# Kernel optimization log

Hardware: AMD Instinct MI355X
Metric: run time of the kernel (lower is better)

The kernel has to match this reference:

```python
import jax, jax.numpy as jnp
import numpy as np

EPS = 1e-6      # torch F.pairwise_distance default eps (added to the difference)
MARGIN = 1.0

def _cdist_eps(a, b):
    # Exact ||a_i - b_j + eps||_2 via expansion:
    # ||a-b+eps||^2 = ||a||^2 + ||b||^2 - 2 a.b + 2*eps*(sum(a)-sum(b)) + D*eps^2
    D = a.shape[-1]
    sq = (jnp.sum(a * a, axis=1)[:, None]
          + jnp.sum(b * b, axis=1)[None, :]
          - 2.0 * (a @ b.T)
          + 2.0 * EPS * (jnp.sum(a, axis=1)[:, None] - jnp.sum(b, axis=1)[None, :])
          + D * EPS * EPS)
    return jnp.sqrt(jnp.maximum(sq, 0.0))

def setup_inputs() -> dict:
    key = jax.random.key(0)
    k1, k2, k3 = jax.random.split(key, 3)
    B, D = 4096, 1024
    return {
        'anchor_embeddings': jax.random.normal(k1, (B, D), dtype=jnp.float32),
        'positive_embeddings': jax.random.normal(k2, (B, D), dtype=jnp.float32),
        'negative_embeddings': jax.random.normal(k3, (B, D), dtype=jnp.float32),
    }

def reference(anchor_embeddings, positive_embeddings, negative_embeddings):
    a, p, n = anchor_embeddings, positive_embeddings, negative_embeddings
    # per-row anchor-positive and anchor-negative distances
    d_ap = jnp.linalg.norm(a - p + EPS, axis=-1)          # [B]
    d_an_row = jnp.linalg.norm(a - n + EPS, axis=-1)      # [B]

    # hardest negative: for each anchor, max over negatives with dist < d_ap[i], else 0
    dan_mat = _cdist_eps(a, n)                            # [B, B]
    mask_n = dan_mat < d_ap[:, None]
    hard_n = jnp.where(mask_n.any(axis=1),
                       jnp.max(jnp.where(mask_n, dan_mat, -jnp.inf), axis=1),
                       0.0)
    d_an = jnp.mean(hard_n)                               # scalar

    # hardest positive: for each anchor, min over positives with dist > d(a_i, n_i), else 0
    dpp_mat = _cdist_eps(a, p)                            # [B, B]
    mask_p = dpp_mat > d_an_row[:, None]
    hard_p = jnp.where(mask_p.any(axis=1),
                       jnp.min(jnp.where(mask_p, dpp_mat, jnp.inf), axis=1),
                       0.0)
    d_pp = jnp.mean(hard_p)                               # scalar

    loss = jnp.mean(jnp.clip(d_ap - 0.5 * d_pp - 0.5 * d_an + MARGIN, 0.0, None))
    return loss
```

## Files before the change

kernel.cpp:

```cpp
#include <hip/hip_runtime.h>


#define NB 4096
#define DIM 1024
#define EPSF 1e-6f
#define D_EPS2 (1024.0f * 1e-6f * 1e-6f)

#define BM 128
#define BK 64

typedef __bf16  bf16x8 __attribute__((ext_vector_type(8)));
typedef float   f32x4  __attribute__((ext_vector_type(4)));

__device__ __forceinline__ unsigned short f2bf(float x) {
    unsigned u = __float_as_uint(x);
    u += 0x7FFFu + ((u >> 16) & 1u);
    return (unsigned short)(u >> 16);
}

__device__ __forceinline__ void g2l16(const unsigned short* g, unsigned short* l) {
    __builtin_amdgcn_global_load_lds(
        (const __attribute__((address_space(1))) unsigned int*)g,
        (__attribute__((address_space(3))) unsigned int*)l, 16, 0, 0);
}


__global__ __launch_bounds__(256) void row_stats_kernel(
    const float* __restrict__ a, const float* __restrict__ p,
    const float* __restrict__ n,
    unsigned short* __restrict__ abf, unsigned short* __restrict__ pbf,
    unsigned short* __restrict__ nbf, float* __restrict__ stats)
{
    const int t    = threadIdx.x;
    const int wave = t >> 6, lane = t & 63;
    const int row  = blockIdx.x * 4 + wave;
    const size_t base = (size_t)row * DIM;

    const float4* a4 = (const float4*)(a + base);
    const float4* p4 = (const float4*)(p + base);
    const float4* n4 = (const float4*)(n + base);

    float v[8] = {0,0,0,0,0,0,0,0};
#pragma unroll
    for (int c = 0; c < 4; c++) {
        const int idx = c * 64 + lane;
        const float4 va = a4[idx];
        const float4 vp = p4[idx];
        const float4 vn = n4[idx];
        const float fa[4] = {va.x, va.y, va.z, va.w};
        const float fp[4] = {vp.x, vp.y, vp.z, vp.w};
        const float fn[4] = {vn.x, vn.y, vn.z, vn.w};
#pragma unroll
        for (int e = 0; e < 4; e++) {
            v[0] += fa[e];           v[1] += fa[e] * fa[e];
            v[2] += fp[e];           v[3] += fp[e] * fp[e];
            v[4] += fn[e];           v[5] += fn[e] * fn[e];
            float dp = fa[e] - fp[e] + EPSF;  v[6] += dp * dp;
            float dn = fa[e] - fn[e] + EPSF;  v[7] += dn * dn;
        }
        ushort4 ba, bp, bn;
        ba.x = f2bf(fa[0]); ba.y = f2bf(fa[1]); ba.z = f2bf(fa[2]); ba.w = f2bf(fa[3]);
        bp.x = f2bf(fp[0]); bp.y = f2bf(fp[1]); bp.z = f2bf(fp[2]); bp.w = f2bf(fp[3]);
        bn.x = f2bf(fn[0]); bn.y = f2bf(fn[1]); bn.z = f2bf(fn[2]); bn.w = f2bf(fn[3]);
        ((ushort4*)(abf + base))[idx] = ba;
        ((ushort4*)(pbf + base))[idx] = bp;
        ((ushort4*)(nbf + base))[idx] = bn;
    }

#pragma unroll
    for (int m = 32; m >= 1; m >>= 1)
#pragma unroll
        for (int q = 0; q < 8; q++) v[q] += __shfl_xor(v[q], m);

    if (lane == 0) {
        stats[0 * NB + row] = v[1] + 2.0f * EPSF * v[0] + D_EPS2;
        stats[1 * NB + row] = v[5] - 2.0f * EPSF * v[4];
        stats[2 * NB + row] = v[3] - 2.0f * EPSF * v[2];
        stats[3 * NB + row] = sqrtf(v[6]);
        stats[4 * NB + row] = sqrtf(v[7]);
        ((unsigned*)stats)[5 * NB + row] = 0u;
        ((unsigned*)stats)[6 * NB + row] = 0x7f800000u;
    }
}

__global__ __launch_bounds__(256, 2) void gemm_mask_kernel(
    const unsigned short* __restrict__ Abf,
    const unsigned short* __restrict__ Nbf,
    const unsigned short* __restrict__ Pbf,
    float* __restrict__ stats)
{
    const int i0 = blockIdx.x * BM;
    const int j0 = blockIdx.y * BM;

    __shared__ unsigned short sA[BM * BK];
    __shared__ unsigned short sN[BM * BK];
    __shared__ unsigned short sP[BM * BK];

    const int t    = threadIdx.x;
    const int wave = t >> 6, lane = t & 63;
    const int wm   = wave >> 1, wn = wave & 1;
    const int quad = lane >> 4, lrow = lane & 15;

    const int srow = lane >> 3;
    const int kch  = ((lane & 7) ^ srow) * 8;
    const unsigned short* gA = Abf + (size_t)(i0 + wave * 32 + srow) * DIM + kch;
    const unsigned short* gN = Nbf + (size_t)(j0 + wave * 32 + srow) * DIM + kch;
    const unsigned short* gP = Pbf + (size_t)(j0 + wave * 32 + srow) * DIM + kch;
    unsigned short* lA = sA + (wave * 32) * BK;
    unsigned short* lN = sN + (wave * 32) * BK;
    unsigned short* lP = sP + (wave * 32) * BK;

    const int rsw0 = ((0 * 4 + quad) ^ (lrow & 7)) * 8;
    const int rsw1 = ((1 * 4 + quad) ^ (lrow & 7)) * 8;
    const unsigned short* pa  = sA + (wm * 64 + lrow) * BK;
    const unsigned short* pbn = sN + (wn * 64 + lrow) * BK;
    const unsigned short* pbp = sP + (wn * 64 + lrow) * BK;

    f32x4 accN[4][4], accP[4][4];
#pragma unroll
    for (int im = 0; im < 4; im++)
#pragma unroll
        for (int jn = 0; jn < 4; jn++) {
            accN[im][jn] = (f32x4)(0.0f);
            accP[im][jn] = (f32x4)(0.0f);
        }

    for (int kt = 0; kt < DIM; kt += BK) {
        __syncthreads();
#pragma unroll
        for (int g = 0; g < 4; g++) {
            g2l16(gA + (size_t)kt + g * 8 * DIM, lA + g * 8 * BK);
            g2l16(gN + (size_t)kt + g * 8 * DIM, lN + g * 8 * BK);
            g2l16(gP + (size_t)kt + g * 8 * DIM, lP + g * 8 * BK);
        }
        __syncthreads();

#pragma unroll
        for (int half = 0; half < 2; half++) {
            const int rsw = half ? rsw1 : rsw0;
            bf16x8 afr[4], bn_fr[4], bp_fr[4];
#pragma unroll
            for (int im = 0; im < 4; im++)
                afr[im] = *(const bf16x8*)(pa + im * 16 * BK + rsw);
#pragma unroll
            for (int jn = 0; jn < 4; jn++) {
                bn_fr[jn] = *(const bf16x8*)(pbn + jn * 16 * BK + rsw);
                bp_fr[jn] = *(const bf16x8*)(pbp + jn * 16 * BK + rsw);
            }
#pragma unroll
            for (int im = 0; im < 4; im++)
#pragma unroll
                for (int jn = 0; jn < 4; jn++) {
                    accN[im][jn] = __builtin_amdgcn_mfma_f32_16x16x32_bf16(
                        afr[im], bn_fr[jn], accN[im][jn], 0, 0, 0);
                    accP[im][jn] = __builtin_amdgcn_mfma_f32_16x16x32_bf16(
                        afr[im], bp_fr[jn], accP[im][jn], 0, 0, 0);
                }
        }
    }

    const float* __restrict__ base_a = stats + 0 * NB;
    const float* __restrict__ cn_v   = stats + 1 * NB;
    const float* __restrict__ cp_v   = stats + 2 * NB;
    const float* __restrict__ d_ap   = stats + 3 * NB;
    const float* __restrict__ d_an   = stats + 4 * NB;
    unsigned* __restrict__ hard_n = ((unsigned*)stats) + 5 * NB;
    unsigned* __restrict__ hard_p = ((unsigned*)stats) + 6 * NB;

#pragma unroll
    for (int im = 0; im < 4; im++) {
#pragma unroll
        for (int r = 0; r < 4; r++) {
            const int gi = i0 + wm * 64 + im * 16 + quad * 4 + r;
            const float cutN = d_ap[gi];
            const float cutP = d_an[gi];
            const float bi   = base_a[gi];
            float bestN = 0.0f;
            float bestP = __uint_as_float(0x7f800000u);
#pragma unroll
            for (int jn = 0; jn < 4; jn++) {
                const int gj = j0 + wn * 64 + jn * 16 + lrow;
                const float dN = sqrtf(fmaxf(bi + cn_v[gj] - 2.0f * accN[im][jn][r], 0.0f));
                const float dP = sqrtf(fmaxf(bi + cp_v[gj] - 2.0f * accP[im][jn][r], 0.0f));
                if (dN < cutN && dN > bestN) bestN = dN;
                if (dP > cutP && dP < bestP) bestP = dP;
            }
#pragma unroll
            for (int m = 1; m < 16; m <<= 1) {
                bestN = fmaxf(bestN, __shfl_xor(bestN, m));
                bestP = fminf(bestP, __shfl_xor(bestP, m));
            }
            if (lrow == 0) {
                const unsigned bn_ = __float_as_uint(bestN);
                const unsigned bp_ = __float_as_uint(bestP);
                if (bn_ != 0u)          atomicMax(hard_n + gi, bn_);
                if (bp_ != 0x7f800000u) atomicMin(hard_p + gi, bp_);
            }
        }
    }
}

__global__ __launch_bounds__(1024) void finalize_kernel(
    const float* __restrict__ stats, float* __restrict__ out)
{
    const unsigned* hard_n = ((const unsigned*)stats) + 5 * NB;
    const unsigned* hard_p = ((const unsigned*)stats) + 6 * NB;
    const float*    d_ap   = stats + 3 * NB;
    const int t = threadIdx.x;
    const int wave = t >> 6, lane = t & 63;
    __shared__ float pn[16], pp[16];
    __shared__ float s_dan, s_dpp;

    float sn = 0.0f, sp = 0.0f;
    for (int i = t; i < NB; i += 1024) {
        sn += __uint_as_float(hard_n[i]);
        const unsigned hp = hard_p[i];
        if (hp != 0x7f800000u) sp += __uint_as_float(hp);
    }
#pragma unroll
    for (int m = 32; m >= 1; m >>= 1) {
        sn += __shfl_xor(sn, m);
        sp += __shfl_xor(sp, m);
    }
    if (lane == 0) { pn[wave] = sn; pp[wave] = sp; }
    __syncthreads();
    if (t == 0) {
        float an = 0.0f, ap = 0.0f;
#pragma unroll
        for (int w = 0; w < 16; w++) { an += pn[w]; ap += pp[w]; }
        s_dan = an / (float)NB;
        s_dpp = ap / (float)NB;
    }
    __syncthreads();
    const float dan = s_dan, dpp = s_dpp;

    float accv = 0.0f;
    for (int i = t; i < NB; i += 1024)
        accv += fmaxf(d_ap[i] - 0.5f * dpp - 0.5f * dan + 1.0f, 0.0f);
#pragma unroll
    for (int m = 32; m >= 1; m >>= 1) accv += __shfl_xor(accv, m);
    if (lane == 0) pn[wave] = accv;
    __syncthreads();
    if (t == 0) {
        float s = 0.0f;
#pragma unroll
        for (int w = 0; w < 16; w++) s += pn[w];
        out[0] = s / (float)NB;
    }
}

extern "C" void kernel_launch(void* const* d_in, const int* in_sizes, int n_in,
                              void* d_out, int out_size, void* d_ws, size_t ws_size,
                              hipStream_t stream) {
    const float* a = (const float*)d_in[0];
    const float* p = (const float*)d_in[1];
    const float* n = (const float*)d_in[2];
    float* out = (float*)d_out;

    unsigned short* abf = (unsigned short*)d_ws;
    unsigned short* pbf = abf + (size_t)NB * DIM;
    unsigned short* nbf = pbf + (size_t)NB * DIM;
    float* stats = (float*)(nbf + (size_t)NB * DIM);

    row_stats_kernel<<<NB / 4, 256, 0, stream>>>(a, p, n, abf, pbf, nbf, stats);

    dim3 grid(NB / BM, NB / BM);
    gemm_mask_kernel<<<grid, 256, 0, stream>>>(abf, nbf, pbf, stats);

    finalize_kernel<<<1, 1024, 0, stream>>>(stats, out);
}
```

Measured before the change: 183.4 us.

## Split fused N/P GEMM into separate blocks, load A directly, compare squared distances

The fused kernel that computed both anchor-negative and anchor-positive accumulators per block is split so that each block handles only one of N or P, selected by a new grid dimension. This halves the accumulator registers and LDS per block and raises the launch-bounds occupancy target. The A fragments are now loaded straight from global memory into registers instead of being staged through LDS. Masking compares squared distances against squared cutoffs, and the sqrt moves into finalize. The costs are A being read twice, uncoalesced global loads of A, and possible rounding differences at the threshold from comparing squares.

```diff
diff --git a/kernel.cpp b/kernel.cpp
--- a/kernel.cpp
+++ b/kernel.cpp
@@ -83,18 +83,18 @@
     }
 }
 
-__global__ __launch_bounds__(256, 2) void gemm_mask_kernel(
+__global__ __launch_bounds__(256, 3) void gemm_mask_kernel(
     const unsigned short* __restrict__ Abf,
     const unsigned short* __restrict__ Nbf,
     const unsigned short* __restrict__ Pbf,
     float* __restrict__ stats)
 {
-    const int i0 = blockIdx.x * BM;
-    const int j0 = blockIdx.y * BM;
-
-    __shared__ unsigned short sA[BM * BK];
-    __shared__ unsigned short sN[BM * BK];
-    __shared__ unsigned short sP[BM * BK];
+    const int  isP = blockIdx.x;
+    const int  j0  = blockIdx.y * BM;
+    const int  i0  = blockIdx.z * BM;
+    const unsigned short* __restrict__ Bmat = isP ? Pbf : Nbf;
+
+    __shared__ unsigned short sB[BM * BK];
 
     const int t    = threadIdx.x;
     const int wave = t >> 6, lane = t & 63;
@@ -103,98 +103,82 @@
 
     const int srow = lane >> 3;
     const int kch  = ((lane & 7) ^ srow) * 8;
-    const unsigned short* gA = Abf + (size_t)(i0 + wave * 32 + srow) * DIM + kch;
-    const unsigned short* gN = Nbf + (size_t)(j0 + wave * 32 + srow) * DIM + kch;
-    const unsigned short* gP = Pbf + (size_t)(j0 + wave * 32 + srow) * DIM + kch;
-    unsigned short* lA = sA + (wave * 32) * BK;
-    unsigned short* lN = sN + (wave * 32) * BK;
-    unsigned short* lP = sP + (wave * 32) * BK;
-
-    const int rsw0 = ((0 * 4 + quad) ^ (lrow & 7)) * 8;
-    const int rsw1 = ((1 * 4 + quad) ^ (lrow & 7)) * 8;
-    const unsigned short* pa  = sA + (wm * 64 + lrow) * BK;
-    const unsigned short* pbn = sN + (wn * 64 + lrow) * BK;
-    const unsigned short* pbp = sP + (wn * 64 + lrow) * BK;
-
-    f32x4 accN[4][4], accP[4][4];
+    const unsigned short* gB = Bmat + (size_t)(j0 + wave * 32 + srow) * DIM + kch;
+    unsigned short* lB = sB + (wave * 32) * BK;
+
+    const unsigned short* gA = Abf + (size_t)(i0 + wm * 64 + lrow) * DIM + (quad << 3);
+
+    const int rsw0 = ((0 + quad) ^ (lrow & 7)) * 8;
+    const int rsw1 = ((4 + quad) ^ (lrow & 7)) * 8;
+    const unsigned short* pb = sB + (wn * 64 + lrow) * BK;
+
+    f32x4 acc[4][4];
 #pragma unroll
     for (int im = 0; im < 4; im++)
 #pragma unroll
-        for (int jn = 0; jn < 4; jn++) {
-            accN[im][jn] = (f32x4)(0.0f);
-            accP[im][jn] = (f32x4)(0.0f);
-        }
+        for (int jn = 0; jn < 4; jn++) acc[im][jn] = (f32x4)(0.0f);
 
     for (int kt = 0; kt < DIM; kt += BK) {
         __syncthreads();
 #pragma unroll
-        for (int g = 0; g < 4; g++) {
-            g2l16(gA + (size_t)kt + g * 8 * DIM, lA + g * 8 * BK);
-            g2l16(gN + (size_t)kt + g * 8 * DIM, lN + g * 8 * BK);
-            g2l16(gP + (size_t)kt + g * 8 * DIM, lP + g * 8 * BK);
-        }
+        for (int g = 0; g < 4; g++)
+            g2l16(gB + (size_t)kt + g * 8 * DIM, lB + g * 8 * BK);
+
+        bf16x8 afr[2][4];
+#pragma unroll
+        for (int h = 0; h < 2; h++)
+#pragma unroll
+            for (int im = 0; im < 4; im++)
+                afr[h][im] = *(const bf16x8*)(gA + kt + h * 32 + im * 16 * DIM);
+
         __syncthreads();
 
 #pragma unroll
         for (int half = 0; half < 2; half++) {
             const int rsw = half ? rsw1 : rsw0;
-            bf16x8 afr[4], bn_fr[4], bp_fr[4];
+            bf16x8 bfr[4];
+#pragma unroll
+            for (int jn = 0; jn < 4; jn++)
+                bfr[jn] = *(const bf16x8*)(pb + jn * 16 * BK + rsw);
 #pragma unroll
             for (int im = 0; im < 4; im++)
-                afr[im] = *(const bf16x8*)(pa + im * 16 * BK + rsw);
-#pragma unroll
-            for (int jn = 0; jn < 4; jn++) {
-                bn_fr[jn] = *(const bf16x8*)(pbn + jn * 16 * BK + rsw);
-                bp_fr[jn] = *(const bf16x8*)(pbp + jn * 16 * BK + rsw);
-            }
-#pragma unroll
-            for (int im = 0; im < 4; im++)
-#pragma unroll
-                for (int jn = 0; jn < 4; jn++) {
-                    accN[im][jn] = __builtin_amdgcn_mfma_f32_16x16x32_bf16(
-                        afr[im], bn_fr[jn], accN[im][jn], 0, 0, 0);
-                    accP[im][jn] = __builtin_amdgcn_mfma_f32_16x16x32_bf16(
-                        afr[im], bp_fr[jn], accP[im][jn], 0, 0, 0);
-                }
+#pragma unroll
+                for (int jn = 0; jn < 4; jn++)
+                    acc[im][jn] = __builtin_amdgcn_mfma_f32_16x16x32_bf16(
+                        afr[half][im], bfr[jn], acc[im][jn], 0, 0, 0);
         }
     }
 
     const float* __restrict__ base_a = stats + 0 * NB;
-    const float* __restrict__ cn_v   = stats + 1 * NB;
-    const float* __restrict__ cp_v   = stats + 2 * NB;
-    const float* __restrict__ d_ap   = stats + 3 * NB;
-    const float* __restrict__ d_an   = stats + 4 * NB;
-    unsigned* __restrict__ hard_n = ((unsigned*)stats) + 5 * NB;
-    unsigned* __restrict__ hard_p = ((unsigned*)stats) + 6 * NB;
+    const float* __restrict__ c_v    = isP ? (stats + 2 * NB) : (stats + 1 * NB);
+    const float* __restrict__ cut_v  = isP ? (stats + 4 * NB) : (stats + 3 * NB);
+    unsigned* __restrict__ hard = ((unsigned*)stats) + (isP ? 6 : 5) * NB;
 
 #pragma unroll
     for (int im = 0; im < 4; im++) {
 #pragma unroll
         for (int r = 0; r < 4; r++) {
             const int gi = i0 + wm * 64 + im * 16 + quad * 4 + r;
-            const float cutN = d_ap[gi];
-            const float cutP = d_an[gi];
+            const float cut  = cut_v[gi];
+            const float cut2 = cut * cut;
             const float bi   = base_a[gi];
-            float bestN = 0.0f;
-            float bestP = __uint_as_float(0x7f800000u);
+            float best = isP ? __uint_as_float(0x7f800000u) : 0.0f;
 #pragma unroll
             for (int jn = 0; jn < 4; jn++) {
                 const int gj = j0 + wn * 64 + jn * 16 + lrow;
-                const float dN = sqrtf(fmaxf(bi + cn_v[gj] - 2.0f * accN[im][jn][r], 0.0f));
-                const float dP = sqrtf(fmaxf(bi + cp_v[gj] - 2.0f * accP[im][jn][r], 0.0f));
-                if (dN < cutN && dN > bestN) bestN = dN;
-                if (dP > cutP && dP < bestP) bestP = dP;
+                const float sq = fmaxf(bi + c_v[gj] - 2.0f * acc[im][jn][r], 0.0f);
+                if (isP) { if (sq > cut2 && sq < best) best = sq; }
+                else     { if (sq < cut2 && sq > best) best = sq; }
             }
 #pragma unroll
             for (int m = 1; m < 16; m <<= 1) {
-                bestN = fmaxf(bestN, __shfl_xor(bestN, m));
-                bestP = fminf(bestP, __shfl_xor(bestP, m));
+                float o = __shfl_xor(best, m);
+                best = isP ? fminf(best, o) : fmaxf(best, o);
             }
             if (lrow == 0) {
-                const unsigned bn_ = __float_as_uint(bestN);
-                const unsigned bp_ = __float_as_uint(bestP);
-                if (bn_ != 0u)          atomicMax(hard_n + gi, bn_);
-                if (bp_ != 0x7f800000u) atomicMin(hard_p + gi, bp_);
+                const unsigned bits = __float_as_uint(best);
+                if (isP) { if (bits != 0x7f800000u) atomicMin(hard + gi, bits); }
+                else     { if (bits != 0u)          atomicMax(hard + gi, bits); }
             }
         }
     }
@@ -213,9 +197,9 @@
 
     float sn = 0.0f, sp = 0.0f;
     for (int i = t; i < NB; i += 1024) {
-        sn += __uint_as_float(hard_n[i]);
+        sn += sqrtf(__uint_as_float(hard_n[i]));
         const unsigned hp = hard_p[i];
-        if (hp != 0x7f800000u) sp += __uint_as_float(hp);
+        if (hp != 0x7f800000u) sp += sqrtf(__uint_as_float(hp));
     }
 #pragma unroll
     for (int m = 32; m >= 1; m >>= 1) {
@@ -264,7 +248,7 @@
 
     row_stats_kernel<<<NB / 4, 256, 0, stream>>>(a, p, n, abf, pbf, nbf, stats);
 
-    dim3 grid(NB / BM, NB / BM);
+    dim3 grid(2, NB / BM, NB / BM);
     gemm_mask_kernel<<<grid, 256, 0, stream>>>(abf, nbf, pbf, stats);
 
     finalize_kernel<<<1, 1024, 0, stream>>>(stats, out);
```

After: 259.6 us. 1.42x slower.

## Double-buffer N/P tiles in LDS, load A fragments directly to registers

Applied to the files above, without the earlier changes.

Rewrites the GEMM main loop as a two-stage software pipeline: N and P tiles are double-buffered in LDS with async global-to-LDS loads, synchronised by explicit vmcnt waits and barriers. The A operand now skips LDS and is loaded straight from global into register fragments. The epilogue compares squared distances against squared cutoffs and defers the sqrt to the finalize kernel. The aim is to hide load latency and remove the per-iteration double barrier and A-tile LDS traffic, at the cost of more registers (occupancy hint removed) and a hand-tuned waitcnt scheme.

```diff
diff --git a/kernel.cpp b/kernel.cpp
--- a/kernel.cpp
+++ b/kernel.cpp
@@ -23,6 +23,12 @@
         (const __attribute__((address_space(1))) unsigned int*)g,
         (__attribute__((address_space(3))) unsigned int*)l, 16, 0, 0);
 }
+
+#define FENCE      asm volatile("" ::: "memory")
+#define WAITVM16   asm volatile("s_waitcnt vmcnt(16)" ::: "memory")
+#define WAITVM0    asm volatile("s_waitcnt vmcnt(0)" ::: "memory")
+#define BARRIER    asm volatile("s_barrier" ::: "memory")
+#define BARRIER_LG asm volatile("s_waitcnt lgkmcnt(0)\n\ts_barrier" ::: "memory")
 
 
 __global__ __launch_bounds__(256) void row_stats_kernel(
@@ -83,18 +89,17 @@
     }
 }
 
-__global__ __launch_bounds__(256, 2) void gemm_mask_kernel(
+__global__ __launch_bounds__(256) void gemm_mask_kernel(
     const unsigned short* __restrict__ Abf,
     const unsigned short* __restrict__ Nbf,
     const unsigned short* __restrict__ Pbf,
     float* __restrict__ stats)
 {
-    const int i0 = blockIdx.x * BM;
-    const int j0 = blockIdx.y * BM;
-
-    __shared__ unsigned short sA[BM * BK];
-    __shared__ unsigned short sN[BM * BK];
-    __shared__ unsigned short sP[BM * BK];
+    const int j0 = blockIdx.x * BM;
+    const int i0 = blockIdx.y * BM;
+
+    __shared__ unsigned short sN[2][BM * BK];
+    __shared__ unsigned short sP[2][BM * BK];
 
     const int t    = threadIdx.x;
     const int wave = t >> 6, lane = t & 63;
@@ -103,19 +108,17 @@
 
     const int srow = lane >> 3;
     const int kch  = ((lane & 7) ^ srow) * 8;
-    const unsigned short* gA = Abf + (size_t)(i0 + wave * 32 + srow) * DIM + kch;
     const unsigned short* gN = Nbf + (size_t)(j0 + wave * 32 + srow) * DIM + kch;
     const unsigned short* gP = Pbf + (size_t)(j0 + wave * 32 + srow) * DIM + kch;
-    unsigned short* lA = sA + (wave * 32) * BK;
-    unsigned short* lN = sN + (wave * 32) * BK;
-    unsigned short* lP = sP + (wave * 32) * BK;
-
-    const int rsw0 = ((0 * 4 + quad) ^ (lrow & 7)) * 8;
-    const int rsw1 = ((1 * 4 + quad) ^ (lrow & 7)) * 8;
-    const unsigned short* pa  = sA + (wm * 64 + lrow) * BK;
-    const unsigned short* pbn = sN + (wn * 64 + lrow) * BK;
-    const unsigned short* pbp = sP + (wn * 64 + lrow) * BK;
-
+    const int lbase = (wave * 32) * BK;
+
+    const unsigned short* gA = Abf + (size_t)(i0 + wm * 64 + lrow) * DIM + (quad << 3);
+
+    const int rsw0 = ((0 + quad) ^ (lrow & 7)) * 8;
+    const int rsw1 = ((4 + quad) ^ (lrow & 7)) * 8;
+    const int pboff = (wn * 64 + lrow) * BK;
+
+    bf16x8 afr[2][2][4];
     f32x4 accN[4][4], accP[4][4];
 #pragma unroll
     for (int im = 0; im < 4; im++)
@@ -125,39 +128,73 @@
             accP[im][jn] = (f32x4)(0.0f);
         }
 
-    for (int kt = 0; kt < DIM; kt += BK) {
-        __syncthreads();
-#pragma unroll
-        for (int g = 0; g < 4; g++) {
-            g2l16(gA + (size_t)kt + g * 8 * DIM, lA + g * 8 * BK);
-            g2l16(gN + (size_t)kt + g * 8 * DIM, lN + g * 8 * BK);
-            g2l16(gP + (size_t)kt + g * 8 * DIM, lP + g * 8 * BK);
-        }
-        __syncthreads();
-
-#pragma unroll
-        for (int half = 0; half < 2; half++) {
-            const int rsw = half ? rsw1 : rsw0;
-            bf16x8 afr[4], bn_fr[4], bp_fr[4];
-#pragma unroll
-            for (int im = 0; im < 4; im++)
-                afr[im] = *(const bf16x8*)(pa + im * 16 * BK + rsw);
-#pragma unroll
-            for (int jn = 0; jn < 4; jn++) {
-                bn_fr[jn] = *(const bf16x8*)(pbn + jn * 16 * BK + rsw);
-                bp_fr[jn] = *(const bf16x8*)(pbp + jn * 16 * BK + rsw);
-            }
-#pragma unroll
-            for (int im = 0; im < 4; im++)
-#pragma unroll
-                for (int jn = 0; jn < 4; jn++) {
-                    accN[im][jn] = __builtin_amdgcn_mfma_f32_16x16x32_bf16(
-                        afr[im], bn_fr[jn], accN[im][jn], 0, 0, 0);
-                    accP[im][jn] = __builtin_amdgcn_mfma_f32_16x16x32_bf16(
-                        afr[im], bp_fr[jn], accP[im][jn], 0, 0, 0);
-                }
-        }
-    }
+#define ISSUE(kw_, b_) do {                                                   \
+    const unsigned short* _gn = gN + (size_t)(kw_) * BK;                      \
+    const unsigned short* _gp = gP + (size_t)(kw_) * BK;                      \
+    unsigned short* _ln = &sN[(b_)][lbase];                                   \
+    unsigned short* _lp = &sP[(b_)][lbase];                                   \
+    _Pragma("unroll")                                                         \
+    for (int g = 0; g < 4; g++) {                                             \
+        g2l16(_gn + (size_t)g * 8 * DIM, _ln + g * 8 * BK);                   \
+        g2l16(_gp + (size_t)g * 8 * DIM, _lp + g * 8 * BK);                   \
+    }                                                                         \
+    const unsigned short* _ga = gA + (size_t)(kw_) * BK;                      \
+    _Pragma("unroll")                                                         \
+    for (int h = 0; h < 2; h++)                                               \
+        _Pragma("unroll")                                                     \
+        for (int im = 0; im < 4; im++)                                        \
+            afr[(b_)][h][im] = *(const bf16x8*)(_ga + h * 32 + im * 16 * DIM);\
+} while (0)
+
+#define COMPUTE(b_) do {                                                      \
+    _Pragma("unroll")                                                         \
+    for (int half = 0; half < 2; half++) {                                    \
+        const int rsw = half ? rsw1 : rsw0;                                   \
+        bf16x8 bnfr[4], bpfr[4];                                              \
+        _Pragma("unroll")                                                     \
+        for (int jn = 0; jn < 4; jn++) {                                      \
+            bnfr[jn] = *(const bf16x8*)(&sN[(b_)][pboff + jn * 16 * BK + rsw]);\
+            bpfr[jn] = *(const bf16x8*)(&sP[(b_)][pboff + jn * 16 * BK + rsw]);\
+        }                                                                     \
+        _Pragma("unroll")                                                     \
+        for (int im = 0; im < 4; im++)                                        \
+            _Pragma("unroll")                                                 \
+            for (int jn = 0; jn < 4; jn++) {                                  \
+                accN[im][jn] = __builtin_amdgcn_mfma_f32_16x16x32_bf16(       \
+                    afr[(b_)][half][im], bnfr[jn], accN[im][jn], 0, 0, 0);    \
+                accP[im][jn] = __builtin_amdgcn_mfma_f32_16x16x32_bf16(       \
+                    afr[(b_)][half][im], bpfr[jn], accP[im][jn], 0, 0, 0);    \
+            }                                                                 \
+    }                                                                         \
+} while (0)
+
+    ISSUE(0, 0);
+    FENCE;
+    ISSUE(1, 1);
+    WAITVM16;
+    BARRIER;
+
+    for (int kp = 0; kp < 7; kp++) {
+        COMPUTE(0);
+        BARRIER_LG;
+        ISSUE(2 * kp + 2, 0);
+        WAITVM16;
+        BARRIER;
+
+        COMPUTE(1);
+        BARRIER_LG;
+        ISSUE(2 * kp + 3, 1);
+        WAITVM16;
+        BARRIER;
+    }
+    COMPUTE(0);
+    BARRIER_LG;
+    WAITVM0;
+    BARRIER;
+    COMPUTE(1);
+
+#undef COMPUTE
+#undef ISSUE
 
     const float* __restrict__ base_a = stats + 0 * NB;
     const float* __restrict__ cn_v   = stats + 1 * NB;
@@ -174,16 +211,18 @@
             const int gi = i0 + wm * 64 + im * 16 + quad * 4 + r;
             const float cutN = d_ap[gi];
             const float cutP = d_an[gi];
-            const float bi   = base_a[gi];
+            const float cutN2 = cutN * cutN;
+            const float cutP2 = cutP * cutP;
+            const float bi    = base_a[gi];
             float bestN = 0.0f;
             float bestP = __uint_as_float(0x7f800000u);
 #pragma unroll
             for (int jn = 0; jn < 4; jn++) {
                 const int gj = j0 + wn * 64 + jn * 16 + lrow;
-                const float dN = sqrtf(fmaxf(bi + cn_v[gj] - 2.0f * accN[im][jn][r], 0.0f));
-                const float dP = sqrtf(fmaxf(bi + cp_v[gj] - 2.0f * accP[im][jn][r], 0.0f));
-                if (dN < cutN && dN > bestN) bestN = dN;
-                if (dP > cutP && dP < bestP) bestP = dP;
+                const float sqN = fmaxf(bi + cn_v[gj] - 2.0f * accN[im][jn][r], 0.0f);
+                const float sqP = fmaxf(bi + cp_v[gj] - 2.0f * accP[im][jn][r], 0.0f);
+                if (sqN < cutN2 && sqN > bestN) bestN = sqN;
+                if (sqP > cutP2 && sqP < bestP) bestP = sqP;
             }
 #pragma unroll
             for (int m = 1; m < 16; m <<= 1) {
@@ -213,9 +252,9 @@
 
     float sn = 0.0f, sp = 0.0f;
     for (int i = t; i < NB; i += 1024) {
-        sn += __uint_as_float(hard_n[i]);
+        sn += sqrtf(__uint_as_float(hard_n[i]));
         const unsigned hp = hard_p[i];
-        if (hp != 0x7f800000u) sp += __uint_as_float(hp);
+        if (hp != 0x7f800000u) sp += sqrtf(__uint_as_float(hp));
     }
 #pragma unroll
     for (int m = 32; m >= 1; m >>= 1) {
```

Result: slower. 250.8 us (+36.8%).

## Load anchor fragments from global into registers; compare squared distances in epilogue

Applied to the files above, without the earlier changes.

Drops the shared-memory staging of the anchor tile: each lane now loads its A MFMA fragments straight from global memory into registers, and the grid mapping is swapped so blocks sharing an anchor row tile sit next to each other. The epilogue compares squared distances against squared cutoffs and defers the sqrt to the finalize kernel, removing per-element sqrt calls. The MFMA loop is reordered to load B fragments per column, which lowers register pressure. The risks are uncoalesced global loads of A with more global traffic and latency not hidden by LDS, and slight changes at the mask boundary from comparing squared values.

```diff
diff --git a/kernel.cpp b/kernel.cpp
--- a/kernel.cpp
+++ b/kernel.cpp
@@ -89,10 +89,9 @@
     const unsigned short* __restrict__ Pbf,
     float* __restrict__ stats)
 {
-    const int i0 = blockIdx.x * BM;
-    const int j0 = blockIdx.y * BM;
-
-    __shared__ unsigned short sA[BM * BK];
+    const int j0 = blockIdx.x * BM;
+    const int i0 = blockIdx.y * BM;
+
     __shared__ unsigned short sN[BM * BK];
     __shared__ unsigned short sP[BM * BK];
 
@@ -103,16 +102,15 @@
 
     const int srow = lane >> 3;
     const int kch  = ((lane & 7) ^ srow) * 8;
-    const unsigned short* gA = Abf + (size_t)(i0 + wave * 32 + srow) * DIM + kch;
     const unsigned short* gN = Nbf + (size_t)(j0 + wave * 32 + srow) * DIM + kch;
     const unsigned short* gP = Pbf + (size_t)(j0 + wave * 32 + srow) * DIM + kch;
-    unsigned short* lA = sA + (wave * 32) * BK;
     unsigned short* lN = sN + (wave * 32) * BK;
     unsigned short* lP = sP + (wave * 32) * BK;
 
-    const int rsw0 = ((0 * 4 + quad) ^ (lrow & 7)) * 8;
-    const int rsw1 = ((1 * 4 + quad) ^ (lrow & 7)) * 8;
-    const unsigned short* pa  = sA + (wm * 64 + lrow) * BK;
+    const unsigned short* gA = Abf + (size_t)(i0 + wm * 64 + lrow) * DIM + (quad << 3);
+
+    const int rsw0 = ((0 + quad) ^ (lrow & 7)) * 8;
+    const int rsw1 = ((4 + quad) ^ (lrow & 7)) * 8;
     const unsigned short* pbn = sN + (wn * 64 + lrow) * BK;
     const unsigned short* pbp = sP + (wn * 64 + lrow) * BK;
 
@@ -129,33 +127,33 @@
         __syncthreads();
 #pragma unroll
         for (int g = 0; g < 4; g++) {
-            g2l16(gA + (size_t)kt + g * 8 * DIM, lA + g * 8 * BK);
             g2l16(gN + (size_t)kt + g * 8 * DIM, lN + g * 8 * BK);
             g2l16(gP + (size_t)kt + g * 8 * DIM, lP + g * 8 * BK);
         }
+        bf16x8 afr[2][4];
+#pragma unroll
+        for (int h = 0; h < 2; h++)
+#pragma unroll
+            for (int im = 0; im < 4; im++)
+                afr[h][im] = *(const bf16x8*)(gA + kt + h * 32 + im * 16 * DIM);
+
         __syncthreads();
 
 #pragma unroll
         for (int half = 0; half < 2; half++) {
             const int rsw = half ? rsw1 : rsw0;
-            bf16x8 afr[4], bn_fr[4], bp_fr[4];
-#pragma unroll
-            for (int im = 0; im < 4; im++)
-                afr[im] = *(const bf16x8*)(pa + im * 16 * BK + rsw);
 #pragma unroll
             for (int jn = 0; jn < 4; jn++) {
-                bn_fr[jn] = *(const bf16x8*)(pbn + jn * 16 * BK + rsw);
-                bp_fr[jn] = *(const bf16x8*)(pbp + jn * 16 * BK + rsw);
-            }
-#pragma unroll
-            for (int im = 0; im < 4; im++)
-#pragma unroll
-                for (int jn = 0; jn < 4; jn++) {
+                const bf16x8 bnfr = *(const bf16x8*)(pbn + jn * 16 * BK + rsw);
+                const bf16x8 bpfr = *(const bf16x8*)(pbp + jn * 16 * BK + rsw);
+#pragma unroll
+                for (int im = 0; im < 4; im++) {
                     accN[im][jn] = __builtin_amdgcn_mfma_f32_16x16x32_bf16(
-                        afr[im], bn_fr[jn], accN[im][jn], 0, 0, 0);
+                        afr[half][im], bnfr, accN[im][jn], 0, 0, 0);
                     accP[im][jn] = __builtin_amdgcn_mfma_f32_16x16x32_bf16(
-                        afr[im], bp_fr[jn], accP[im][jn], 0, 0, 0);
+                        afr[half][im], bpfr, accP[im][jn], 0, 0, 0);
                 }
+            }
         }
     }
 
@@ -174,16 +172,18 @@
             const int gi = i0 + wm * 64 + im * 16 + quad * 4 + r;
             const float cutN = d_ap[gi];
             const float cutP = d_an[gi];
-            const float bi   = base_a[gi];
+            const float cutN2 = cutN * cutN;
+            const float cutP2 = cutP * cutP;
+            const float bi    = base_a[gi];
             float bestN = 0.0f;
             float bestP = __uint_as_float(0x7f800000u);
 #pragma unroll
             for (int jn = 0; jn < 4; jn++) {
                 const int gj = j0 + wn * 64 + jn * 16 + lrow;
-                const float dN = sqrtf(fmaxf(bi + cn_v[gj] - 2.0f * accN[im][jn][r], 0.0f));
-                const float dP = sqrtf(fmaxf(bi + cp_v[gj] - 2.0f * accP[im][jn][r], 0.0f));
-                if (dN < cutN && dN > bestN) bestN = dN;
-                if (dP > cutP && dP < bestP) bestP = dP;
+                const float sqN = fmaxf(bi + cn_v[gj] - 2.0f * accN[im][jn][r], 0.0f);
+                const float sqP = fmaxf(bi + cp_v[gj] - 2.0f * accP[im][jn][r], 0.0f);
+                if (sqN < cutN2 && sqN > bestN) bestN = sqN;
+                if (sqP > cutP2 && sqP < bestP) bestP = sqP;
             }
 #pragma unroll
             for (int m = 1; m < 16; m <<= 1) {
@@ -213,9 +213,9 @@
 
     float sn = 0.0f, sp = 0.0f;
     for (int i = t; i < NB; i += 1024) {
-        sn += __uint_as_float(hard_n[i]);
+        sn += sqrtf(__uint_as_float(hard_n[i]));
         const unsigned hp = hard_p[i];
-        if (hp != 0x7f800000u) sp += __uint_as_float(hp);
+        if (hp != 0x7f800000u) sp += sqrtf(__uint_as_float(hp));
     }
 #pragma unroll
     for (int m = 32; m >= 1; m >>= 1) {
```

Measured after the change: 197.1 us. 7.5% more time.
